# Kernel optimization log

Hardware: AMD Instinct MI355X
Metric: run time of the kernel (lower is better)

Reference implementation:

```python
import jax, jax.numpy as jnp
import numpy as np

# Contact model constants (from ContactModel defaults / hardcoded values)
STIFFNESS = 100000.0
DISSIPATION = 0.2
STATIC_FRICTION = 0.8
DYNAMIC_FRICTION = 0.8
VISCOUS_FRICTION = 0.5
TRANSITION_VELOCITY = 0.2
GROUND_HEIGHT = 0.0
DT = 0.05
RADIUS = 0.032
EPS = 1e-5
EPS2 = 1e-16
BV = 50.0
BD = 300.0

# 12 spheres: 6 right (bodies 4,5), 6 left (bodies 9,10)
SPHERE_BODY = np.array([4, 4, 4, 4, 5, 5, 9, 9, 9, 9, 10, 10], dtype=np.int32)
SPHERE_LOCAL = np.array([
    [0.00190115788407966, -0.01, -0.00382630379623308],
    [0.148386399942063,   -0.01, -0.028713422052654],
    [0.133001170607051,   -0.01,  0.0516362473449566],
    [0.0662346661991635,  -0.01,  0.0263641606741698],
    [0.06,                -0.01, -0.0187603084619177],
    [0.045,               -0.01,  0.0618569567549652],
    [0.00190115788407966, -0.01,  0.00382630379623308],
    [0.148386399942063,   -0.01,  0.028713422052654],
    [0.133001170607051,   -0.01, -0.0516362473449566],
    [0.0662346661991635,  -0.01, -0.0263641606741698],
    [0.06,                -0.01,  0.0187603084619177],
    [0.045,               -0.01, -0.0618569567549652],
], dtype=np.float32)
NORMAL = np.array([0.0, 1.0, 0.0], dtype=np.float32)


def _sphere_positions(joints, joints_ori):
    # joints: (B,24,3), joints_ori: (B,24,3,3) -> (B,12,3)
    body_pos = joints[:, SPHERE_BODY]            # (B,12,3)
    body_ori = joints_ori[:, SPHERE_BODY]        # (B,12,3,3)
    local = jnp.asarray(SPHERE_LOCAL)
    return body_pos + jnp.einsum('bsij,sj->bsi', body_ori, local)


def _contact_forces(pos, vel):
    # pos, vel: (B,S,3) -> forces (B,S,3); fully vectorized over spheres
    n = jnp.asarray(NORMAL)
    indentation = GROUND_HEIGHT - pos[..., 1]                    # (B,S)
    vnormal = vel[..., 1]                                        # dot(vel, [0,1,0])
    vtangent = vel - vnormal[..., None] * n                      # (B,S,3)
    ind_vel = -vnormal
    k = 0.5 * STIFFNESS ** (2.0 / 3.0)
    # sqrt(ind^2+eps)**1.5 == (ind^2+eps)**0.75
    fH = (4.0 / 3.0) * k * np.sqrt(RADIUS * k) * (indentation * indentation + EPS) ** 0.75
    fHd = fH * (1.0 + 1.5 * DISSIPATION * ind_vel)
    fn = ((0.5 * jnp.tanh(BV * (ind_vel + 1.0 / (1.5 * DISSIPATION))) + 0.5 + EPS2)
          * (0.5 * jnp.tanh(BD * indentation) + 0.5 + EPS2) * fHd)
    vslip = jnp.sqrt(jnp.sum(vtangent * vtangent, axis=-1) + EPS)
    vrel = vslip / TRANSITION_VELOCITY
    ffriction = fn * (jnp.minimum(vrel, 1.0)
                      * (DYNAMIC_FRICTION + 2.0 * (STATIC_FRICTION - DYNAMIC_FRICTION) / (1.0 + vrel * vrel))
                      + VISCOUS_FRICTION * vslip)
    force = fn[..., None] * n
    friction_force = ffriction[..., None] * (-vtangent) / (vslip[..., None] + EPS)
    return force + friction_force


def _cop_and_torque(pos, forces):
    # pos, forces: (B,S,3) -> cop (B,3), torque (B,3); vectorized batch version of the per-b loop
    vf = forces[..., 1]                          # (B,S)
    valid = vf > 0.0
    w = jnp.where(valid, vf, 0.0)
    tw = jnp.sum(w, axis=-1)                     # (B,)
    has = tw > 0.0
    tw_safe = jnp.where(has, tw, 1.0)
    cop_x = jnp.where(has, jnp.sum(pos[..., 0] * w, axis=-1) / tw_safe, 0.0)
    cop_y = jnp.where(has, GROUND_HEIGHT, 0.0)
    cop_z = jnp.where(has, jnp.sum(pos[..., 2] * w, axis=-1) / tw_safe, 0.0)
    cop = jnp.stack([cop_x, cop_y, cop_z], axis=-1)  # (B,3)
    r = pos - cop[:, None, :]
    f_masked = jnp.where(valid[..., None], forces, 0.0)  # only valid contacts contribute torque
    torque = jnp.sum(jnp.cross(r, f_masked), axis=1)
    return cop, torque


def setup_inputs() -> dict:
    key = jax.random.key(0)
    k1, k2 = jax.random.split(key)
    B = 262144
    joints = jax.random.normal(k1, (B, 24, 3), dtype=jnp.float32)
    joints_ori = jax.random.normal(k2, (B, 24, 3, 3), dtype=jnp.float32)
    return {"joints": joints, "joints_ori": joints_ori}


def reference(joints, joints_ori):
    pos = _sphere_positions(joints, joints_ori)              # (B,12,3)
    # finite-difference sphere velocity over frames (dt); zero at first frame
    vel = (pos - jnp.concatenate([pos[:1], pos[:-1]], axis=0)) / DT
    sphere_forces = _contact_forces(pos, vel)                # (B,12,3)

    force = jnp.sum(sphere_forces, axis=1)
    force_right = jnp.sum(sphere_forces[:, :6], axis=1)
    force_left = jnp.sum(sphere_forces[:, 6:], axis=1)
    cop, torque = _cop_and_torque(pos, sphere_forces)
    cop_right, torque_right = _cop_and_torque(pos[:, :6], sphere_forces[:, :6])
    cop_left, torque_left = _cop_and_torque(pos[:, 6:], sphere_forces[:, 6:])
    return (force, torque, cop, sphere_forces, pos,
            force_right, force_left, torque_right, torque_left, cop_right, cop_left)
```

## Files before the change

kernel.cpp:

```cpp
#include <hip/hip_runtime.h>
#include <math.h>


__global__ __launch_bounds__(256)
void contact_kernel(const float* __restrict__ joints,
                    const float* __restrict__ jori,
                    float* __restrict__ out, const int B)
{
    const int lane = threadIdx.x & 63;
    const int wg   = blockIdx.x * 4 + (threadIdx.x >> 6);
    const long bL  = (long)wg * 63 + lane;
    const bool do_write = (bL < B) && (lane > 0 || bL == 0);
    const int  b = (bL < (long)B) ? (int)bL : (B - 1);

    float px[12], py[12], pz[12];
    float fx[12], fy[12], fz[12];

    {
        const float c_lx[12] = {0.00190115788407966f, 0.148386399942063f, 0.133001170607051f,
                                0.0662346661991635f, 0.06f, 0.045f,
                                0.00190115788407966f, 0.148386399942063f, 0.133001170607051f,
                                0.0662346661991635f, 0.06f, 0.045f};
        const float c_lz[12] = {-0.00382630379623308f, -0.028713422052654f, 0.0516362473449566f,
                                 0.0263641606741698f, -0.0187603084619177f, 0.0618569567549652f,
                                 0.00382630379623308f, 0.028713422052654f, -0.0516362473449566f,
                                -0.0263641606741698f, 0.0187603084619177f, -0.0618569567549652f};
        const float ly = -0.01f;
        const int bodies[4] = {4, 5, 9, 10};
        const int sbeg[4]   = {0, 4, 6, 10};
        const int scnt[4]   = {4, 2, 4, 2};
        const float* jr = joints + (size_t)b * 72;
        const float* mr = jori   + (size_t)b * 216;
        #pragma unroll
        for (int bi = 0; bi < 4; ++bi) {
            const int body = bodies[bi];
            const float jx = jr[body*3+0], jy = jr[body*3+1], jz = jr[body*3+2];
            const float* m = mr + body*9;
            const float m00=m[0],m01=m[1],m02=m[2];
            const float m10=m[3],m11=m[4],m12=m[5];
            const float m20=m[6],m21=m[7],m22=m[8];
            #pragma unroll
            for (int si = 0; si < 4; ++si) {
                if (si < scnt[bi]) {
                    const int s = sbeg[bi] + si;
                    const float lx = c_lx[s], lz = c_lz[s];
                    px[s] = jx + m00*lx + m01*ly + m02*lz;
                    py[s] = jy + m10*lx + m11*ly + m12*lz;
                    pz[s] = jz + m20*lx + m21*ly + m22*lz;
                }
            }
        }
    }

    #pragma unroll
    for (int s = 0; s < 12; ++s) {
        fx[s] = (px[s] - __shfl_up(px[s], 1)) * 20.0f;
        fy[s] = (py[s] - __shfl_up(py[s], 1)) * 20.0f;
        fz[s] = (pz[s] - __shfl_up(pz[s], 1)) * 20.0f;
    }

    const float KF  = 1077.21734501594f;
    const float CFH = (4.0f/3.0f) * KF * sqrtf(0.032f * KF);
    #pragma unroll
    for (int s = 0; s < 12; ++s) {
        const float vx = fx[s], vy = fy[s], vz = fz[s];
        const float ind     = -py[s];
        const float ind_vel = -vy;
        const float q   = ind*ind + 1e-5f;
        const float fH  = CFH * sqrtf(q * sqrtf(q));
        const float fHd = fH * (1.0f + 0.3f * ind_vel);
        const float t1 = (0.5f*tanhf(50.0f*(ind_vel + 3.3333333333333335f)) + 0.5f) + 1e-16f;
        const float t2 = (0.5f*tanhf(300.0f*ind) + 0.5f) + 1e-16f;
        const float fn = t1 * t2 * fHd;
        const float vslip = sqrtf(vx*vx + vz*vz + 1e-5f);
        const float vrel  = vslip * 5.0f;
        const float mu  = fminf(vrel, 1.0f) * 0.8f + 0.5f * vslip;
        const float ffr = fn * mu;
        const float sc  = ffr / (vslip + 1e-5f);
        fx[s] = -sc * vx;
        fy[s] = fn;
        fz[s] = -sc * vz;
    }

    float res[3][9];
    const int gs0[3] = {0, 0, 6};
    const int gs1[3] = {12, 6, 12};
    #pragma unroll
    for (int g = 0; g < 3; ++g) {
        float Fx=0.f, Fy=0.f, Fz=0.f, tw=0.f, sx=0.f, sz=0.f;
        #pragma unroll
        for (int s = 0; s < 12; ++s) {
            if (s >= gs0[g] && s < gs1[g]) {
                Fx += fx[s]; Fy += fy[s]; Fz += fz[s];
                const float w = fy[s] > 0.f ? fy[s] : 0.f;
                tw += w;
                sx += px[s] * w;
                sz += pz[s] * w;
            }
        }
        const bool has = tw > 0.f;
        const float cx = has ? sx / tw : 0.f;
        const float cz = has ? sz / tw : 0.f;
        float Tx=0.f, Ty=0.f, Tz=0.f;
        #pragma unroll
        for (int s = 0; s < 12; ++s) {
            if (s >= gs0[g] && s < gs1[g]) {
                if (fy[s] > 0.f) {
                    const float rx = px[s]-cx, ry = py[s], rz = pz[s]-cz;
                    Tx += ry*fz[s] - rz*fy[s];
                    Ty += rz*fx[s] - rx*fz[s];
                    Tz += rx*fy[s] - ry*fx[s];
                }
            }
        }
        res[g][0]=Fx; res[g][1]=Fy; res[g][2]=Fz;
        res[g][3]=Tx; res[g][4]=Ty; res[g][5]=Tz;
        res[g][6]=cx; res[g][7]=0.f; res[g][8]=cz;
    }

    if (do_write) {
        const size_t sB = (size_t)B;
        const size_t t3 = (size_t)b * 3;
        float* o;
        o = out;           o[t3]=res[0][0]; o[t3+1]=res[0][1]; o[t3+2]=res[0][2];
        o = out + sB*3;    o[t3]=res[0][3]; o[t3+1]=res[0][4]; o[t3+2]=res[0][5];
        o = out + sB*6;    o[t3]=res[0][6]; o[t3+1]=res[0][7]; o[t3+2]=res[0][8];
        o = out + sB*81;   o[t3]=res[1][0]; o[t3+1]=res[1][1]; o[t3+2]=res[1][2];
        o = out + sB*84;   o[t3]=res[2][0]; o[t3+1]=res[2][1]; o[t3+2]=res[2][2];
        o = out + sB*87;   o[t3]=res[1][3]; o[t3+1]=res[1][4]; o[t3+2]=res[1][5];
        o = out + sB*90;   o[t3]=res[2][3]; o[t3+1]=res[2][4]; o[t3+2]=res[2][5];
        o = out + sB*93;   o[t3]=res[1][6]; o[t3+1]=res[1][7]; o[t3+2]=res[1][8];
        o = out + sB*96;   o[t3]=res[2][6]; o[t3+1]=res[2][7]; o[t3+2]=res[2][8];

        float* osf = out + sB*9  + (size_t)b*36;
        float* opp = out + sB*45 + (size_t)b*36;
        if ((B & 3) == 0) {
            float bufF[36], bufP[36];
            #pragma unroll
            for (int s = 0; s < 12; ++s) {
                bufF[s*3+0]=fx[s]; bufF[s*3+1]=fy[s]; bufF[s*3+2]=fz[s];
                bufP[s*3+0]=px[s]; bufP[s*3+1]=py[s]; bufP[s*3+2]=pz[s];
            }
            #pragma unroll
            for (int i = 0; i < 9; ++i) {
                reinterpret_cast<float4*>(osf)[i] = reinterpret_cast<float4*>(bufF)[i];
                reinterpret_cast<float4*>(opp)[i] = reinterpret_cast<float4*>(bufP)[i];
            }
        } else {
            #pragma unroll
            for (int s = 0; s < 12; ++s) {
                osf[s*3+0]=fx[s]; osf[s*3+1]=fy[s]; osf[s*3+2]=fz[s];
                opp[s*3+0]=px[s]; opp[s*3+1]=py[s]; opp[s*3+2]=pz[s];
            }
        }
    }
}

extern "C" void kernel_launch(void* const* d_in, const int* in_sizes, int n_in,
                              void* d_out, int out_size, void* d_ws, size_t ws_size,
                              hipStream_t stream) {
    const float* joints = (const float*)d_in[0];
    const float* jori   = (const float*)d_in[1];
    float* out = (float*)d_out;
    const int B = in_sizes[0] / 72;
    long waves = ((long)B + 61) / 63;
    if (waves < 1) waves = 1;
    const int blocks = (int)((waves + 3) / 4);
    contact_kernel<<<blocks, 256, 0, stream>>>(joints, jori, out, B);
}
```

Before: 69.93 us.

## Stage needed joint rows in LDS with halo and recompute previous-frame positions

The kernel now loads only the four bodies' positions and orientations into shared memory, cooperatively across each block, including one halo row from the previous frame. Each thread then recomputes the previous frame's sphere positions from LDS instead of using wave shuffles. This removes the 63-of-64-lane wave layout and its wasted lanes, and turns strided per-thread global reads into block-cooperative reads. In exchange it adds about 50 KB of LDS per block, which limits occupancy, plus a block-wide barrier and duplicated position arithmetic.

```diff
diff --git a/kernel.cpp b/kernel.cpp
--- a/kernel.cpp
+++ b/kernel.cpp
@@ -7,11 +7,46 @@
                     const float* __restrict__ jori,
                     float* __restrict__ out, const int B)
 {
-    const int lane = threadIdx.x & 63;
-    const int wg   = blockIdx.x * 4 + (threadIdx.x >> 6);
-    const long bL  = (long)wg * 63 + lane;
-    const bool do_write = (bL < B) && (lane > 0 || bL == 0);
-    const int  b = (bL < (long)B) ? (int)bL : (B - 1);
+    __shared__ float lds[257 * 49];
+    const int tid = threadIdx.x;
+    const long B0 = (long)blockIdx.x * 256;
+
+    #pragma unroll 2
+    for (int idx = tid; idx < 257 * 6; idx += 256) {
+        const int r = idx / 6, c = idx - r * 6;
+        long br = B0 - 1 + r;
+        br = br < 0 ? 0 : (br >= B ? B - 1 : br);
+        lds[r * 49 + c] = joints[br * 72 + 12 + c];
+    }
+    #pragma unroll 2
+    for (int idx = tid; idx < 257 * 6; idx += 256) {
+        const int r = idx / 6, c = idx - r * 6;
+        long br = B0 - 1 + r;
+        br = br < 0 ? 0 : (br >= B ? B - 1 : br);
+        lds[r * 49 + 6 + c] = joints[br * 72 + 27 + c];
+    }
+    #pragma unroll 2
+    for (int idx = tid; idx < 257 * 18; idx += 256) {
+        const int r = idx / 18, c = idx - r * 18;
+        long br = B0 - 1 + r;
+        br = br < 0 ? 0 : (br >= B ? B - 1 : br);
+        lds[r * 49 + 12 + c] = jori[br * 216 + 36 + c];
+    }
+    #pragma unroll 2
+    for (int idx = tid; idx < 257 * 18; idx += 256) {
+        const int r = idx / 18, c = idx - r * 18;
+        long br = B0 - 1 + r;
+        br = br < 0 ? 0 : (br >= B ? B - 1 : br);
+        lds[r * 49 + 30 + c] = jori[br * 216 + 81 + c];
+    }
+    __syncthreads();
+
+    const long bb = B0 + tid;
+    if (bb >= B) return;
+    const int b = (int)bb;
+
+    const float* own = &lds[(tid + 1) * 49];
+    const float* prv = &lds[tid * 49];
 
     float px[12], py[12], pz[12];
     float fx[12], fy[12], fz[12];
@@ -26,37 +61,40 @@
                                  0.00382630379623308f, 0.028713422052654f, -0.0516362473449566f,
                                 -0.0263641606741698f, 0.0187603084619177f, -0.0618569567549652f};
         const float ly = -0.01f;
-        const int bodies[4] = {4, 5, 9, 10};
-        const int sbeg[4]   = {0, 4, 6, 10};
-        const int scnt[4]   = {4, 2, 4, 2};
-        const float* jr = joints + (size_t)b * 72;
-        const float* mr = jori   + (size_t)b * 216;
+        const int jc[4]   = {0, 3, 6, 9};
+        const int oc[4]   = {12, 21, 30, 39};
+        const int sbeg[4] = {0, 4, 6, 10};
+        const int scnt[4] = {4, 2, 4, 2};
         #pragma unroll
         for (int bi = 0; bi < 4; ++bi) {
-            const int body = bodies[bi];
-            const float jx = jr[body*3+0], jy = jr[body*3+1], jz = jr[body*3+2];
-            const float* m = mr + body*9;
+            const float jx = own[jc[bi]+0], jy = own[jc[bi]+1], jz = own[jc[bi]+2];
+            const float* m = own + oc[bi];
             const float m00=m[0],m01=m[1],m02=m[2];
             const float m10=m[3],m11=m[4],m12=m[5];
             const float m20=m[6],m21=m[7],m22=m[8];
+            const float kx = prv[jc[bi]+0], ky = prv[jc[bi]+1], kz = prv[jc[bi]+2];
+            const float* nn = prv + oc[bi];
+            const float n00=nn[0],n01=nn[1],n02=nn[2];
+            const float n10=nn[3],n11=nn[4],n12=nn[5];
+            const float n20=nn[6],n21=nn[7],n22=nn[8];
             #pragma unroll
             for (int si = 0; si < 4; ++si) {
                 if (si < scnt[bi]) {
                     const int s = sbeg[bi] + si;
                     const float lx = c_lx[s], lz = c_lz[s];
-                    px[s] = jx + m00*lx + m01*ly + m02*lz;
-                    py[s] = jy + m10*lx + m11*ly + m12*lz;
-                    pz[s] = jz + m20*lx + m21*ly + m22*lz;
+                    const float ax = jx + m00*lx + m01*ly + m02*lz;
+                    const float ay = jy + m10*lx + m11*ly + m12*lz;
+                    const float az = jz + m20*lx + m21*ly + m22*lz;
+                    const float bx = kx + n00*lx + n01*ly + n02*lz;
+                    const float by = ky + n10*lx + n11*ly + n12*lz;
+                    const float bz = kz + n20*lx + n21*ly + n22*lz;
+                    px[s] = ax; py[s] = ay; pz[s] = az;
+                    fx[s] = (ax - bx) * 20.0f;
+                    fy[s] = (ay - by) * 20.0f;
+                    fz[s] = (az - bz) * 20.0f;
                 }
             }
         }
-    }
-
-    #pragma unroll
-    for (int s = 0; s < 12; ++s) {
-        fx[s] = (px[s] - __shfl_up(px[s], 1)) * 20.0f;
-        fy[s] = (py[s] - __shfl_up(py[s], 1)) * 20.0f;
-        fz[s] = (pz[s] - __shfl_up(pz[s], 1)) * 20.0f;
     }
 
     const float KF  = 1077.21734501594f;
@@ -118,7 +156,7 @@
         res[g][6]=cx; res[g][7]=0.f; res[g][8]=cz;
     }
 
-    if (do_write) {
+    {
         const size_t sB = (size_t)B;
         const size_t t3 = (size_t)b * 3;
         float* o;
@@ -163,8 +201,7 @@
     const float* jori   = (const float*)d_in[1];
     float* out = (float*)d_out;
     const int B = in_sizes[0] / 72;
-    long waves = ((long)B + 61) / 63;
-    if (waves < 1) waves = 1;
-    const int blocks = (int)((waves + 3) / 4);
+    int blocks = (B + 255) / 256;
+    if (blocks < 1) blocks = 1;
     contact_kernel<<<blocks, 256, 0, stream>>>(joints, jori, out, B);
 }
```

Measured after the change: 81.32 us. 16.3% more time.
